# Kernel optimization log

Hardware: AMD Instinct MI355X
Metric: run time of the kernel (lower is better)

Reference implementation:

```python
import math
import jax, jax.numpy as jnp
import numpy as np

NUM_HEADS = 4
HEAD_DIM = 384


def reshape_fortran(x, shape):
    # column-major (Fortran) reshape, matching the torch reverse-permute trick
    x = jnp.transpose(x, tuple(reversed(range(x.ndim))))
    x = x.reshape(tuple(reversed(shape)))
    return jnp.transpose(x, tuple(reversed(range(len(shape)))))


def rel_pos_rotate(data):
    # data: [b, n_heads, L=2M-1, S] -> [b, n_heads, S, S]
    data = jnp.transpose(data, (0, 2, 3, 1))  # [b, d0=L, d1=S, d2=H]
    b, d0, d1, d2 = data.shape
    data = jnp.concatenate([data, jnp.zeros((b, d1, d1, d2), data.dtype)], axis=1)
    data = reshape_fortran(data, (b, (d0 + d1) * d1, 1, d2))
    data = data[:, :(d1 + d0 - 1) * d1]
    data = reshape_fortran(data, (b, d0 + d1 - 1, d1, d2))
    n = d0 // 2
    data = jnp.swapaxes(data[:, n:n + d1], 1, 2)  # [b, d1, d1, d2]
    return jnp.transpose(data, (0, 3, 1, 2))      # [b, H, S, S]


def setup_inputs() -> dict:
    key = jax.random.key(0)
    ks = jax.random.split(key, 5)
    B, S, D = 4, 920, 1536
    M = 920
    return {
        "hidden_states": jax.random.normal(ks[0], (B, S, D), jnp.float32),
        "q_w": jax.random.normal(ks[1], (D, NUM_HEADS * HEAD_DIM), jnp.float32) * 0.02,
        "k_w": jax.random.normal(ks[2], (D, NUM_HEADS * HEAD_DIM), jnp.float32) * 0.02,
        "v_w": jax.random.normal(ks[3], (D, NUM_HEADS * HEAD_DIM), jnp.float32) * 0.02,
        "dist_emb": jax.random.normal(ks[4], (2 * M - 1, HEAD_DIM), jnp.float32) * 0.02,
    }


def reference(hidden_states, q_w, k_w, v_w, dist_emb):
    B, S, D = hidden_states.shape

    def heads(x):  # [B,S,H*hd] -> [B,H,S,hd]
        return jnp.transpose(x.reshape(B, S, NUM_HEADS, HEAD_DIM), (0, 2, 1, 3))

    # query is pre-scaled by 1/sqrt(head_dim), matching the torch code
    q = heads((hidden_states @ q_w) / math.sqrt(HEAD_DIM))
    k = heads(hidden_states @ k_w)
    v = heads(hidden_states @ v_w)

    scores = jnp.einsum("bhqd,bhkd->bhqk", q, k)  # [B,H,S,S]
    # relative position scores: [B,H,L,S] then skew-rotated into [B,H,S,S]
    rel = jnp.einsum("ld,bhsd->bhls", dist_emb, q)
    scores = scores + rel_pos_rotate(rel)

    probs = jax.nn.softmax(scores, axis=-1)
    ctx = jnp.einsum("bhqk,bhkd->bhqd", probs, v)  # [B,H,S,hd]
    ctx = jnp.transpose(ctx, (0, 2, 1, 3)).reshape(B, S, NUM_HEADS * HEAD_DIM)
    return ctx
```

## Files before the change

### kernel.cpp

```cpp
#include <hip/hip_runtime.h>
#include <cstdint>
#include <cstddef>

#define SEQ   920
#define DM    1536
#define DH    384
#define NHD   4
#define NB    4
#define NBH   16
#define MTOK  3680
#define NREL  1839

typedef short          bf16x8 __attribute__((ext_vector_type(8)));
typedef float          f32x4  __attribute__((ext_vector_type(4)));
typedef unsigned short u16x4  __attribute__((ext_vector_type(4)));
typedef unsigned short u16x8  __attribute__((ext_vector_type(8)));

__device__ __forceinline__ unsigned short f2bf(float f){
  union{float f; unsigned u;} v; v.f = f;
  unsigned r = v.u + 0x7FFFu + ((v.u >> 16) & 1u);
  return (unsigned short)(r >> 16);
}
__device__ __forceinline__ float bf2f(unsigned short h){
  union{unsigned u; float f;} v; v.u = ((unsigned)h) << 16;
  return v.f;
}
__device__ __forceinline__ f32x4 mfma_bf16(bf16x8 a, bf16x8 b, f32x4 c){
  return __builtin_amdgcn_mfma_f32_16x16x32_bf16(a, b, c, 0, 0, 0);
}
__device__ __forceinline__ void gload_lds16(const void* g, void* l){
  __builtin_amdgcn_global_load_lds((const __attribute__((address_space(1))) void*)g,
                                   (__attribute__((address_space(3))) void*)l, 16, 0, 0);
}

__global__ __launch_bounds__(256) void k_prep(const float* __restrict__ X,
                                              const float* __restrict__ de,
                                              const float* __restrict__ qw,
                                              const float* __restrict__ kw,
                                              const float* __restrict__ vw,
                                              unsigned short* __restrict__ Xb,
                                              unsigned short* __restrict__ Eb,
                                              unsigned short* __restrict__ Wt){
  __shared__ float t[32][33];
  int bid = blockIdx.x;
  if(bid < 6912){
    int z = bid / 2304, rem = bid % 2304;
    int k0 = (rem % 48) * 32, n0 = (rem / 48) * 32;
    const float* w = z == 0 ? qw : (z == 1 ? kw : vw);
    int tx = threadIdx.x & 31, ty = threadIdx.x >> 5;
    #pragma unroll
    for(int j = 0; j < 4; j++)
      t[ty*4+j][tx] = w[(size_t)(k0 + ty*4 + j) * DM + n0 + tx];
    __syncthreads();
    #pragma unroll
    for(int j = 0; j < 4; j++)
      Wt[(size_t)(z*DM + n0 + ty*4 + j) * DM + k0 + tx] = f2bf(t[tx][ty*4+j]);
  } else if(bid < 6912 + 2048){
    int i = ((bid - 6912) * 256 + threadIdx.x) * 4;
    const int n = MTOK*DM, stride = 2048 * 256 * 4;
    for(; i + 3 < n; i += stride){
      f32x4 v = *(const f32x4*)(X + i);
      u16x4 o; o.x = f2bf(v.x); o.y = f2bf(v.y); o.z = f2bf(v.z); o.w = f2bf(v.w);
      *(u16x4*)(Xb + i) = o;
    }
  } else {
    int i = ((bid - 6912 - 2048) * 256 + threadIdx.x) * 4;
    if(i + 3 < NREL*DH){
      f32x4 v = *(const f32x4*)(de + i);
      u16x4 o; o.x = f2bf(v.x); o.y = f2bf(v.y); o.z = f2bf(v.z); o.w = f2bf(v.w);
      *(u16x4*)(Eb + i) = o;
    }
  }
}

template<class Epi>
__device__ __forceinline__ void gemm384(const unsigned short* __restrict__ A, int lda, int Amax,
                                        const unsigned short* __restrict__ B, int ldb, int Bmax,
                                        int K, int m0, int n0, Epi epi){
  __shared__ char lds[147456];
  char* ldsA = lds;
  char* ldsB = lds + 98304;
  const int tid = threadIdx.x;
  const int w = tid >> 6, l = tid & 63;
  const int lg = l >> 4, lo = l & 15;
  const int wm = w >> 1, wn = w & 1;

  const int gcol = ((tid & 7) ^ ((tid >> 3) & 7)) * 16;
  const char* gA[6]; const char* gB[3];
  #pragma unroll
  for(int u = 0; u < 6; u++){
    int ar = m0 + u*64 + (tid >> 3); ar = ar < Amax ? ar : Amax - 1;
    gA[u] = (const char*)A + (size_t)ar*lda*2 + gcol;
  }
  #pragma unroll
  for(int v = 0; v < 3; v++){
    int br = n0 + v*64 + (tid >> 3); br = br < Bmax ? br : Bmax - 1;
    gB[v] = (const char*)B + (size_t)br*ldb*2 + gcol;
  }
  auto stA = [&](int kt, int s, int u){
    gload_lds16(gA[u] + (size_t)kt*128, ldsA + s*49152 + u*8192 + tid*16);
  };
  auto stB = [&](int kt, int s, int v){
    gload_lds16(gB[v] + (size_t)kt*128, ldsB + s*24576 + v*8192 + tid*16);
  };

  f32x4 acc[6][6] = {};
  const int sw = (lo & 7) << 4;
  const int nk = K >> 6;

  stA(0,0,0); stA(0,0,1); stA(0,0,3); stA(0,0,4);
  stB(0,0,0); stB(0,0,1); stB(0,0,2);
  stA(0,0,2); stA(0,0,5);
  asm volatile("s_waitcnt vmcnt(2)" ::: "memory");
  __builtin_amdgcn_s_barrier();

  for(int t = 0; t < nk; t++){
    const int s = t & 1, sn = s ^ 1;
    const bool pf = (t + 1 < nk);
    const char* Ab = ldsA + s*49152;
    const char* Bb = ldsB + s*24576;
    bf16x8 bfr[6][2], af[2][2];

    #pragma unroll
    for(int fj = 0; fj < 6; fj++){
      int row = wn*96 + fj*16 + lo;
      #pragma unroll
      for(int kk = 0; kk < 2; kk++)
        bfr[fj][kk] = *(const bf16x8*)(Bb + row*128 + ((kk*64 + lg*16) ^ sw));
    }
    #pragma unroll
    for(int fi = 0; fi < 2; fi++){
      int row = wm*96 + fi*16 + lo;
      #pragma unroll
      for(int kk = 0; kk < 2; kk++)
        af[fi][kk] = *(const bf16x8*)(Ab + row*128 + ((kk*64 + lg*16) ^ sw));
    }
    if(pf){ stA(t+1,sn,0); stA(t+1,sn,1); stA(t+1,sn,3);
            asm volatile("s_waitcnt vmcnt(3)" ::: "memory"); }
    else  { asm volatile("s_waitcnt vmcnt(0)" ::: "memory"); }
    __builtin_amdgcn_s_barrier();
    asm volatile("s_waitcnt lgkmcnt(0)" ::: "memory");
    __builtin_amdgcn_s_setprio(1);
    #pragma unroll
    for(int kk = 0; kk < 2; kk++)
      #pragma unroll
      for(int fi = 0; fi < 2; fi++)
        #pragma unroll
        for(int fj = 0; fj < 6; fj++)
          acc[fi][fj] = mfma_bf16(af[fi][kk], bfr[fj][kk], acc[fi][fj]);
    __builtin_amdgcn_s_setprio(0);

    #pragma unroll
    for(int fi = 0; fi < 2; fi++){
      int row = wm*96 + (fi + 2)*16 + lo;
      #pragma unroll
      for(int kk = 0; kk < 2; kk++)
        af[fi][kk] = *(const bf16x8*)(Ab + row*128 + ((kk*64 + lg*16) ^ sw));
    }
    if(pf){ stA(t+1,sn,4); stB(t+1,sn,0); stB(t+1,sn,1); }
    __builtin_amdgcn_s_barrier();
    asm volatile("s_waitcnt lgkmcnt(0)" ::: "memory");
    __builtin_amdgcn_s_setprio(1);
    #pragma unroll
    for(int kk = 0; kk < 2; kk++)
      #pragma unroll
      for(int fi = 0; fi < 2; fi++)
        #pragma unroll
        for(int fj = 0; fj < 6; fj++)
          acc[fi + 2][fj] = mfma_bf16(af[fi][kk], bfr[fj][kk], acc[fi + 2][fj]);
    __builtin_amdgcn_s_setprio(0);

    #pragma unroll
    for(int fi = 0; fi < 2; fi++){
      int row = wm*96 + (fi + 4)*16 + lo;
      #pragma unroll
      for(int kk = 0; kk < 2; kk++)
        af[fi][kk] = *(const bf16x8*)(Ab + row*128 + ((kk*64 + lg*16) ^ sw));
    }
    if(pf){ stB(t+1,sn,2); stA(t+1,sn,2); stA(t+1,sn,5);
            asm volatile("s_waitcnt vmcnt(2)" ::: "memory"); }
    __builtin_amdgcn_s_barrier();
    asm volatile("s_waitcnt lgkmcnt(0)" ::: "memory");
    __builtin_amdgcn_s_setprio(1);
    #pragma unroll
    for(int kk = 0; kk < 2; kk++)
      #pragma unroll
      for(int fi = 0; fi < 2; fi++)
        #pragma unroll
        for(int fj = 0; fj < 6; fj++)
          acc[fi + 4][fj] = mfma_bf16(af[fi][kk], bfr[fj][kk], acc[fi + 4][fj]);
    __builtin_amdgcn_s_setprio(0);
  }

  #pragma unroll
  for(int fi = 0; fi < 6; fi++)
    #pragma unroll
    for(int fj = 0; fj < 6; fj++){
      int m = m0 + wm*96 + fi*16 + lg*4;
      int n = n0 + wn*96 + fj*16 + lo;
      epi(m, n, acc[fi][fj]);
    }
}

template<class Epi>
__device__ __forceinline__ void gemm192(const unsigned short* __restrict__ A, int lda, int Amax,
                                        const unsigned short* __restrict__ B, int ldb, int Bmax,
                                        int K, int m0, int n0, Epi epi){
  __shared__ unsigned short As[3*192*64];
  __shared__ unsigned short Bs[3*192*64];
  const int tid = threadIdx.x;
  const int w = tid >> 6, l = tid & 63;
  const int lg = l >> 4, lo = l & 15;
  const int wm = w >> 2, wn = w & 3;

  const char* ga[3]; const char* gb[3];
  #pragma unroll
  for(int r = 0; r < 3; r++){
    int row = r*64 + (tid >> 3);
    int gslot = (tid & 7) ^ (row & 7);
    int ar = m0 + row; ar = ar < Amax ? ar : Amax - 1;
    ga[r] = (const char*)A + (size_t)ar*lda*2 + gslot*16;
    int br = n0 + row; br = br < Bmax ? br : Bmax - 1;
    gb[r] = (const char*)B + (size_t)br*ldb*2 + gslot*16;
  }
  const int ldst = tid * 16;

  auto stage_pair = [&](int kt, int slot, int r){
    size_t koff = (size_t)kt * 128;
    gload_lds16(ga[r] + koff, (char*)As + slot*24576 + r*8192 + ldst);
    gload_lds16(gb[r] + koff, (char*)Bs + slot*24576 + r*8192 + ldst);
  };

  f32x4 acc[6][3] = {};
  const int sw = (lo & 7) << 4;
  const int nk = (2*K + 127) >> 7;
  const int tb = 2*K - (nk - 1)*128;
  const bool keep0 = (lg*16) < tb;
  const bool keep1 = (64 + lg*16) < tb;

  #pragma unroll
  for(int r = 0; r < 3; r++) stage_pair(0, 0, r);
  #pragma unroll
  for(int r = 0; r < 3; r++) stage_pair(1, 1, r);
  asm volatile("s_waitcnt vmcnt(6)" ::: "memory");
  __builtin_amdgcn_s_barrier();

  int st = 0;
  for(int t = 0; t < nk; t++){
    const bool last = (t == nk - 1);
    const bool pf = (t + 2 < nk);
    const int s2 = st + 2 >= 3 ? st - 1 : st + 2;
    const char* Ab = (const char*)As + st*24576;
    const char* Bb = (const char*)Bs + st*24576;

    bf16x8 bfr[3][2], afr[2][2];

    #pragma unroll
    for(int fj = 0; fj < 3; fj++){
      int row = wn*48 + fj*16 + lo;
      #pragma unroll
      for(int kk = 0; kk < 2; kk++)
        bfr[fj][kk] = *(const bf16x8*)(Bb + row*128 + ((kk*64 + lg*16) ^ sw));
    }
    #pragma unroll
    for(int fi = 0; fi < 2; fi++){
      int row = wm*96 + fi*16 + lo;
      #pragma unroll
      for(int kk = 0; kk < 2; kk++)
        afr[fi][kk] = *(const bf16x8*)(Ab + row*128 + ((kk*64 + lg*16) ^ sw));
    }
    if(pf) stage_pair(t + 2, s2, 0);
    if(last){
      #pragma unroll
      for(int fi = 0; fi < 2; fi++){
        if(!keep0) afr[fi][0] = bf16x8{};
        if(!keep1) afr[fi][1] = bf16x8{};
      }
    }
    __builtin_amdgcn_s_barrier();
    asm volatile("s_waitcnt lgkmcnt(0)" ::: "memory");
    __builtin_amdgcn_s_setprio(1);
    #pragma unroll
    for(int kk = 0; kk < 2; kk++)
      #pragma unroll
      for(int fi = 0; fi < 2; fi++)
        #pragma unroll
        for(int fj = 0; fj < 3; fj++)
          acc[fi][fj] = mfma_bf16(afr[fi][kk], bfr[fj][kk], acc[fi][fj]);
    __builtin_amdgcn_s_setprio(0);
    __builtin_amdgcn_s_barrier();

    #pragma unroll
    for(int fi = 0; fi < 2; fi++){
      int row = wm*96 + (fi + 2)*16 + lo;
      #pragma unroll
      for(int kk = 0; kk < 2; kk++)
        afr[fi][kk] = *(const bf16x8*)(Ab + row*128 + ((kk*64 + lg*16) ^ sw));
    }
    if(pf) stage_pair(t + 2, s2, 1);
    if(last){
      #pragma unroll
      for(int fi = 0; fi < 2; fi++){
        if(!keep0) afr[fi][0] = bf16x8{};
        if(!keep1) afr[fi][1] = bf16x8{};
      }
    }
    __builtin_amdgcn_s_barrier();
    asm volatile("s_waitcnt lgkmcnt(0)" ::: "memory");
    __builtin_amdgcn_s_setprio(1);
    #pragma unroll
    for(int kk = 0; kk < 2; kk++)
      #pragma unroll
      for(int fi = 0; fi < 2; fi++)
        #pragma unroll
        for(int fj = 0; fj < 3; fj++)
          acc[fi + 2][fj] = mfma_bf16(afr[fi][kk], bfr[fj][kk], acc[fi + 2][fj]);
    __builtin_amdgcn_s_setprio(0);
    __builtin_amdgcn_s_barrier();

    #pragma unroll
    for(int fi = 0; fi < 2; fi++){
      int row = wm*96 + (fi + 4)*16 + lo;
      #pragma unroll
      for(int kk = 0; kk < 2; kk++)
        afr[fi][kk] = *(const bf16x8*)(Ab + row*128 + ((kk*64 + lg*16) ^ sw));
    }
    if(pf){
      stage_pair(t + 2, s2, 2);
      asm volatile("s_waitcnt vmcnt(6)" ::: "memory");
    } else if(t + 1 < nk){
      asm volatile("s_waitcnt vmcnt(0)" ::: "memory");
    }
    if(last){
      #pragma unroll
      for(int fi = 0; fi < 2; fi++){
        if(!keep0) afr[fi][0] = bf16x8{};
        if(!keep1) afr[fi][1] = bf16x8{};
      }
    }
    __builtin_amdgcn_s_barrier();
    asm volatile("s_waitcnt lgkmcnt(0)" ::: "memory");
    __builtin_amdgcn_s_setprio(1);
    #pragma unroll
    for(int kk = 0; kk < 2; kk++)
      #pragma unroll
      for(int fi = 0; fi < 2; fi++)
        #pragma unroll
        for(int fj = 0; fj < 3; fj++)
          acc[fi + 4][fj] = mfma_bf16(afr[fi][kk], bfr[fj][kk], acc[fi + 4][fj]);
    __builtin_amdgcn_s_setprio(0);
    __builtin_amdgcn_s_barrier();

    st = st + 1 >= 3 ? 0 : st + 1;
  }

  #pragma unroll
  for(int fi = 0; fi < 6; fi++)
    #pragma unroll
    for(int fj = 0; fj < 3; fj++){
      int m = m0 + wm*96 + fi*16 + lg*4;
      int n = n0 + wn*48 + fj*16 + lo;
      epi(m, n, acc[fi][fj]);
    }
}

template<class Epi>
__device__ __forceinline__ void gemm256(const unsigned short* __restrict__ A, int lda, int Amax,
                                        const unsigned short* __restrict__ B, int ldb, int Bmax,
                                        int K, int m0, int n0, Epi epi){
  __shared__ char lds[131072];
  char* ldsA = lds;
  char* ldsB = lds + 65536;
  const int tid = threadIdx.x;
  const int w = tid >> 6, l = tid & 63;
  const int lg = l >> 4, lo = l & 15;
  const int wm = w >> 2, wn = w & 3;

  const int gcol = ((tid & 7) ^ ((tid >> 3) & 7)) * 16;
  const char* gA[2][2]; const char* gB[2][2];
  #pragma unroll
  for(int u = 0; u < 2; u++)
    #pragma unroll
    for(int j = 0; j < 2; j++){
      int ar = m0 + u*128 + j*64 + (tid >> 3); ar = ar < Amax ? ar : Amax - 1;
      gA[u][j] = (const char*)A + (size_t)ar*lda*2 + gcol;
      int br = n0 + u*128 + j*64 + (tid >> 3); br = br < Bmax ? br : Bmax - 1;
      gB[u][j] = (const char*)B + (size_t)br*ldb*2 + gcol;
    }
  auto stageA = [&](int kt, int s, int u){
    size_t koff = (size_t)kt * 128;
    #pragma unroll
    for(int j = 0; j < 2; j++)
      gload_lds16(gA[u][j] + koff, ldsA + s*32768 + u*16384 + j*8192 + tid*16);
  };
  auto stageB = [&](int kt, int s, int u){
    size_t koff = (size_t)kt * 128;
    #pragma unroll
    for(int j = 0; j < 2; j++)
      gload_lds16(gB[u][j] + koff, ldsB + s*32768 + u*16384 + j*8192 + tid*16);
  };

  f32x4 acc[2][4][4] = {};
  const int sw = (lo & 7) << 4;
  const int nk = K >> 6;

  stageB(0, 0, 0); stageB(0, 0, 1); stageA(0, 0, 0); stageA(0, 0, 1);
  asm volatile("s_waitcnt vmcnt(2)" ::: "memory");
  __builtin_amdgcn_s_barrier();

  for(int t = 0; t < nk; t++){
    const int s = t & 1, sn = s ^ 1;
    const bool pf = (t + 1 < nk);
    const char* Ab = ldsA + s*32768;
    const char* Bb = ldsB + s*32768;
    bf16x8 b0[4], b1[4], ar[4];

    #pragma unroll
    for(int fj = 0; fj < 4; fj++)
      b0[fj] = *(const bf16x8*)(Bb + (wn*64 + fj*16 + lo)*128 + ((lg*16) ^ sw));
    #pragma unroll
    for(int fi = 0; fi < 4; fi++)
      ar[fi] = *(const bf16x8*)(Ab + (wm*64 + fi*16 + lo)*128 + ((lg*16) ^ sw));
    if(pf) stageB(t + 1, sn, 0);
    __builtin_amdgcn_s_barrier();
    asm volatile("s_waitcnt lgkmcnt(0)" ::: "memory");
    __builtin_amdgcn_s_setprio(1);
    #pragma unroll
    for(int fi = 0; fi < 4; fi++)
      #pragma unroll
      for(int fj = 0; fj < 4; fj++)
        acc[0][fi][fj] = mfma_bf16(ar[fi], b0[fj], acc[0][fi][fj]);
    __builtin_amdgcn_s_setprio(0);

    #pragma unroll
    for(int fj = 0; fj < 4; fj++)
      b1[fj] = *(const bf16x8*)(Bb + (wn*64 + fj*16 + lo)*128 + ((64 + lg*16) ^ sw));
    #pragma unroll
    for(int fi = 0; fi < 4; fi++)
      ar[fi] = *(const bf16x8*)(Ab + (wm*64 + fi*16 + lo)*128 + ((64 + lg*16) ^ sw));
    if(pf){ stageB(t + 1, sn, 1);
            asm volatile("s_waitcnt vmcnt(4)" ::: "memory"); }
    else  { asm volatile("s_waitcnt vmcnt(0)" ::: "memory"); }
    __builtin_amdgcn_s_barrier();
    asm volatile("s_waitcnt lgkmcnt(0)" ::: "memory");
    __builtin_amdgcn_s_setprio(1);
    #pragma unroll
    for(int fi = 0; fi < 4; fi++)
      #pragma unroll
      for(int fj = 0; fj < 4; fj++)
        acc[0][fi][fj] = mfma_bf16(ar[fi], b1[fj], acc[0][fi][fj]);
    __builtin_amdgcn_s_setprio(0);

    #pragma unroll
    for(int fi = 0; fi < 4; fi++)
      ar[fi] = *(const bf16x8*)(Ab + (128 + wm*64 + fi*16 + lo)*128 + ((lg*16) ^ sw));
    if(pf) stageA(t + 1, sn, 0);
    __builtin_amdgcn_s_barrier();
    asm volatile("s_waitcnt lgkmcnt(0)" ::: "memory");
    __builtin_amdgcn_s_setprio(1);
    #pragma unroll
    for(int fi = 0; fi < 4; fi++)
      #pragma unroll
      for(int fj = 0; fj < 4; fj++)
        acc[1][fi][fj] = mfma_bf16(ar[fi], b0[fj], acc[1][fi][fj]);
    __builtin_amdgcn_s_setprio(0);

    #pragma unroll
    for(int fi = 0; fi < 4; fi++)
      ar[fi] = *(const bf16x8*)(Ab + (128 + wm*64 + fi*16 + lo)*128 + ((64 + lg*16) ^ sw));
    if(pf){ stageA(t + 1, sn, 1);
            asm volatile("s_waitcnt vmcnt(2)" ::: "memory"); }
    __builtin_amdgcn_s_barrier();
    asm volatile("s_waitcnt lgkmcnt(0)" ::: "memory");
    __builtin_amdgcn_s_setprio(1);
    #pragma unroll
    for(int fi = 0; fi < 4; fi++)
      #pragma unroll
      for(int fj = 0; fj < 4; fj++)
        acc[1][fi][fj] = mfma_bf16(ar[fi], b1[fj], acc[1][fi][fj]);
    __builtin_amdgcn_s_setprio(0);
  }

  #pragma unroll
  for(int lh = 0; lh < 2; lh++)
    #pragma unroll
    for(int fi = 0; fi < 4; fi++)
      #pragma unroll
      for(int fj = 0; fj < 4; fj++){
        int m = m0 + lh*128 + wm*64 + fi*16 + lg*4;
        int n = n0 + wn*64 + fj*16 + lo;
        epi(m, n, acc[lh][fi][fj]);
      }
}

__global__ __launch_bounds__(512, 2) void k_proj(const unsigned short* __restrict__ X,
                                                 const unsigned short* __restrict__ Wt,
                                                 unsigned short* __restrict__ Qb,
                                                 unsigned short* __restrict__ Kb,
                                                 unsigned short* __restrict__ Vt){
  int bid = blockIdx.x;
  int wg  = (bid & 7) * 30 + (bid >> 3);
  int m0 = (wg % 10) * 384, n0 = (wg / 10) * 192;
  gemm384(X, DM, MTOK, Wt, DM, 3*DM, DM, m0, n0,
    [=] __device__ (int m, int n, f32x4 v4){
      if(m >= MTOK) return;
      int which = n / DM, r = n % DM, h = r / DH, d = r % DH;
      int b = m / SEQ, s = m % SEQ;
      int bh = b * NHD + h;
      if(which == 2){
        u16x4 o;
        o.x = f2bf(v4.x); o.y = f2bf(v4.y); o.z = f2bf(v4.z); o.w = f2bf(v4.w);
        *(u16x4*)(Vt + ((size_t)bh*DH + d)*SEQ + s) = o;
      } else if(which == 0){
        #pragma unroll
        for(int i = 0; i < 4; i++)
          Qb[((size_t)bh*SEQ + s + i)*DH + d] = f2bf(v4[i] * 0.05103103630798287f);
      } else {
        #pragma unroll
        for(int i = 0; i < 4; i++)
          Kb[((size_t)bh*SEQ + s + i)*DH + d] = f2bf(v4[i]);
      }
    });
}

__global__ __launch_bounds__(512) void k_rel(const unsigned short* __restrict__ Qb,
                                             const unsigned short* __restrict__ E,
                                             unsigned short* __restrict__ relS){
  int m0 = blockIdx.x * 192, n0 = blockIdx.y * 192;
  int s0 = m0 % SEQ;
  int qlo = s0, qhi = s0 + 191;
  if(qhi >= SEQ){ qlo = 0; qhi = SEQ - 1; }
  if(n0 + 191 < 919 - qhi || n0 > 1838 - qlo) return;
  gemm192(Qb, DH, NBH*SEQ, E, DH, NREL, DH, m0, n0,
    [=] __device__ (int m, int n, f32x4 v4){
      #pragma unroll
      for(int i = 0; i < 4; i++){
        int mi = m + i;
        if(mi >= NBH*SEQ) continue;
        int q = mi % SEQ;
        int j = n - 919 + q;
        if(j < 0 || j >= SEQ) continue;
        relS[(size_t)mi*SEQ + j] = f2bf(v4[i]);
      }
    });
}

__global__ __launch_bounds__(512, 2) void k_sgemm(const unsigned short* __restrict__ Qb,
                                                  const unsigned short* __restrict__ Kb,
                                                  unsigned short* __restrict__ P,
                                                  float* __restrict__ rs2){
  __shared__ float rsLds[256];
  if(threadIdx.x < 256) rsLds[threadIdx.x] = 0.f;
  int bid = blockIdx.x;
  int wg = (bid & 7) * 32 + (bid >> 3);
  int bh = wg >> 4, r = wg & 15;
  int m0 = (r & 3) * 256, n0 = (r >> 2) * 256;
  const unsigned short* A = Qb + (size_t)bh*SEQ*DH;
  const unsigned short* B = Kb + (size_t)bh*SEQ*DH;
  unsigned short* Pbh = P + (size_t)bh*SEQ*SEQ;
  const int lo = threadIdx.x & 15;
  gemm256(A, DH, SEQ, B, DH, SEQ, DH, m0, n0,
    [=] __device__ (int m, int n, f32x4 v4){
      float s[4];
      #pragma unroll
      for(int i = 0; i < 4; i++){
        int mi = m + i;
        float p = 0.f;
        if(mi < SEQ && n < SEQ){
          size_t off = (size_t)mi*SEQ + n;
          p = __expf(v4[i] + bf2f(Pbh[off]));
          Pbh[off] = f2bf(p);
        }
        s[i] = p;
      }
      #pragma unroll
      for(int i = 0; i < 4; i++){
        float v = s[i];
        v += __shfl_xor(v, 1); v += __shfl_xor(v, 2);
        v += __shfl_xor(v, 4); v += __shfl_xor(v, 8);
        if(lo == 0) atomicAdd(&rsLds[m - m0 + i], v);
      }
    });
  __syncthreads();
  if(threadIdx.x < 256){
    int row = m0 + threadIdx.x;
    if(row < SEQ) rs2[(((size_t)(n0 >> 8))*NBH + bh)*SEQ + row] = rsLds[threadIdx.x];
  }
}

__global__ __launch_bounds__(512) void k_pv(const unsigned short* __restrict__ P,
                                            const unsigned short* __restrict__ Vt,
                                            const float* __restrict__ rs2,
                                            float* __restrict__ out){
  int bid = blockIdx.x;
  int idp = (bid & 7) * 20 + (bid >> 3);
  int bh = idp / 10, r = idp % 10;
  int m0 = (r % 5) * 192, n0 = (r / 5) * 192;
  const unsigned short* A = P  + (size_t)bh*SEQ*SEQ;
  const unsigned short* B = Vt + (size_t)bh*DH*SEQ;
  const int b = bh >> 2, h = bh & 3;
  gemm192(A, SEQ, SEQ, B, SEQ, DH, SEQ, m0, n0,
    [=] __device__ (int m, int n, f32x4 v4){
      #pragma unroll
      for(int i = 0; i < 4; i++){
        int mi = m + i;
        if(mi >= SEQ) continue;
        float den = rs2[(size_t)bh*SEQ + mi]
                  + rs2[((size_t)1*NBH + bh)*SEQ + mi]
                  + rs2[((size_t)2*NBH + bh)*SEQ + mi]
                  + rs2[((size_t)3*NBH + bh)*SEQ + mi];
        out[((size_t)(b*SEQ + mi))*DM + h*DH + n] = v4[i] / den;
      }
    });
}

extern "C" void kernel_launch(void* const* d_in, const int* in_sizes, int n_in,
                              void* d_out, int out_size, void* d_ws, size_t ws_size,
                              hipStream_t stream){
  const float* X  = (const float*)d_in[0];
  const float* qw = (const float*)d_in[1];
  const float* kw = (const float*)d_in[2];
  const float* vw = (const float*)d_in[3];
  const float* de = (const float*)d_in[4];
  float* out = (float*)d_out;
  char* ws = (char*)d_ws;

  unsigned short* Qb   = (unsigned short*)ws;
  unsigned short* Kb   = (unsigned short*)(ws + 11304960);
  unsigned short* Vt   = (unsigned short*)(ws + 22609920);
  unsigned short* relS = (unsigned short*)(ws + 33914880);
  unsigned short* Eb   = (unsigned short*)(ws + 60999680);
  unsigned short* Xb   = (unsigned short*)(ws + 33914880);
  unsigned short* Wt   = (unsigned short*)(ws + 45219840);
  float*          rs2  = (float*)(ws + 60999680);

  k_prep<<<dim3(9650), dim3(256), 0, stream>>>(X, de, qw, kw, vw, Xb, Eb, Wt);
  k_proj<<<dim3(240), dim3(512), 0, stream>>>(Xb, Wt, Qb, Kb, Vt);
  k_rel<<<dim3(77,10), dim3(512), 0, stream>>>(Qb, Eb, relS);
  k_sgemm<<<dim3(256), dim3(512), 0, stream>>>(Qb, Kb, relS, rs2);
  k_pv<<<dim3(160), dim3(512), 0, stream>>>(relS, Vt, rs2, out);
}
```

Measured before the change: 210.2 us.

## Simplify GEMM main loop to bulk prefetch and two MFMA phases

Replaces the three-phase GEMM inner loop, which interleaved partial global-to-LDS prefetches with partial vmcnt waits and barriers, with a simpler schedule. Each iteration now issues every next-tile load up front, then runs two MFMA phases of three A fragments each, and ends with one full vmcnt wait and a barrier. The aim is to cut barrier and synchronisation overhead and give the loads a whole iteration to complete. In exchange it holds more fragment registers live and loses the fine-grained staggering of load issue against compute.

```diff
diff --git a/kernel.cpp b/kernel.cpp
--- a/kernel.cpp
+++ b/kernel.cpp
@@ -97,21 +97,22 @@
     int br = n0 + v*64 + (tid >> 3); br = br < Bmax ? br : Bmax - 1;
     gB[v] = (const char*)B + (size_t)br*ldb*2 + gcol;
   }
-  auto stA = [&](int kt, int s, int u){
-    gload_lds16(gA[u] + (size_t)kt*128, ldsA + s*49152 + u*8192 + tid*16);
-  };
-  auto stB = [&](int kt, int s, int v){
-    gload_lds16(gB[v] + (size_t)kt*128, ldsB + s*24576 + v*8192 + tid*16);
+  auto stage_all = [&](int kt, int s){
+    size_t koff = (size_t)kt * 128;
+    #pragma unroll
+    for(int u = 0; u < 6; u++)
+      gload_lds16(gA[u] + koff, ldsA + s*49152 + u*8192 + tid*16);
+    #pragma unroll
+    for(int v = 0; v < 3; v++)
+      gload_lds16(gB[v] + koff, ldsB + s*24576 + v*8192 + tid*16);
   };
 
   f32x4 acc[6][6] = {};
   const int sw = (lo & 7) << 4;
   const int nk = K >> 6;
 
-  stA(0,0,0); stA(0,0,1); stA(0,0,3); stA(0,0,4);
-  stB(0,0,0); stB(0,0,1); stB(0,0,2);
-  stA(0,0,2); stA(0,0,5);
-  asm volatile("s_waitcnt vmcnt(2)" ::: "memory");
+  stage_all(0, 0);
+  asm volatile("s_waitcnt vmcnt(0)" ::: "memory");
   __builtin_amdgcn_s_barrier();
 
   for(int t = 0; t < nk; t++){
@@ -119,77 +120,54 @@
     const bool pf = (t + 1 < nk);
     const char* Ab = ldsA + s*49152;
     const char* Bb = ldsB + s*24576;
-    bf16x8 bfr[6][2], af[2][2];
-
+    if(pf) stage_all(t + 1, sn);
+
+    bf16x8 b0[6], b1[6], a0[3], a1[3];
     #pragma unroll
     for(int fj = 0; fj < 6; fj++){
-      int row = wn*96 + fj*16 + lo;
-      #pragma unroll
-      for(int kk = 0; kk < 2; kk++)
-        bfr[fj][kk] = *(const bf16x8*)(Bb + row*128 + ((kk*64 + lg*16) ^ sw));
-    }
-    #pragma unroll
-    for(int fi = 0; fi < 2; fi++){
-      int row = wm*96 + fi*16 + lo;
-      #pragma unroll
-      for(int kk = 0; kk < 2; kk++)
-        af[fi][kk] = *(const bf16x8*)(Ab + row*128 + ((kk*64 + lg*16) ^ sw));
-    }
-    if(pf){ stA(t+1,sn,0); stA(t+1,sn,1); stA(t+1,sn,3);
-            asm volatile("s_waitcnt vmcnt(3)" ::: "memory"); }
-    else  { asm volatile("s_waitcnt vmcnt(0)" ::: "memory"); }
-    __builtin_amdgcn_s_barrier();
-    asm volatile("s_waitcnt lgkmcnt(0)" ::: "memory");
-    __builtin_amdgcn_s_setprio(1);
-    #pragma unroll
-    for(int kk = 0; kk < 2; kk++)
-      #pragma unroll
-      for(int fi = 0; fi < 2; fi++)
-        #pragma unroll
-        for(int fj = 0; fj < 6; fj++)
-          acc[fi][fj] = mfma_bf16(af[fi][kk], bfr[fj][kk], acc[fi][fj]);
-    __builtin_amdgcn_s_setprio(0);
-
-    #pragma unroll
-    for(int fi = 0; fi < 2; fi++){
-      int row = wm*96 + (fi + 2)*16 + lo;
-      #pragma unroll
-      for(int kk = 0; kk < 2; kk++)
-        af[fi][kk] = *(const bf16x8*)(Ab + row*128 + ((kk*64 + lg*16) ^ sw));
-    }
-    if(pf){ stA(t+1,sn,4); stB(t+1,sn,0); stB(t+1,sn,1); }
-    __builtin_amdgcn_s_barrier();
-    asm volatile("s_waitcnt lgkmcnt(0)" ::: "memory");
-    __builtin_amdgcn_s_setprio(1);
-    #pragma unroll
-    for(int kk = 0; kk < 2; kk++)
-      #pragma unroll
-      for(int fi = 0; fi < 2; fi++)
-        #pragma unroll
-        for(int fj = 0; fj < 6; fj++)
-          acc[fi + 2][fj] = mfma_bf16(af[fi][kk], bfr[fj][kk], acc[fi + 2][fj]);
-    __builtin_amdgcn_s_setprio(0);
-
-    #pragma unroll
-    for(int fi = 0; fi < 2; fi++){
-      int row = wm*96 + (fi + 4)*16 + lo;
-      #pragma unroll
-      for(int kk = 0; kk < 2; kk++)
-        af[fi][kk] = *(const bf16x8*)(Ab + row*128 + ((kk*64 + lg*16) ^ sw));
-    }
-    if(pf){ stB(t+1,sn,2); stA(t+1,sn,2); stA(t+1,sn,5);
-            asm volatile("s_waitcnt vmcnt(2)" ::: "memory"); }
-    __builtin_amdgcn_s_barrier();
-    asm volatile("s_waitcnt lgkmcnt(0)" ::: "memory");
-    __builtin_amdgcn_s_setprio(1);
-    #pragma unroll
-    for(int kk = 0; kk < 2; kk++)
-      #pragma unroll
-      for(int fi = 0; fi < 2; fi++)
-        #pragma unroll
-        for(int fj = 0; fj < 6; fj++)
-          acc[fi + 4][fj] = mfma_bf16(af[fi][kk], bfr[fj][kk], acc[fi + 4][fj]);
-    __builtin_amdgcn_s_setprio(0);
+      b0[fj] = *(const bf16x8*)(Bb + (wn*96 + fj*16 + lo)*128 + ((lg*16) ^ sw));
+      b1[fj] = *(const bf16x8*)(Bb + (wn*96 + fj*16 + lo)*128 + ((64 + lg*16) ^ sw));
+    }
+    #pragma unroll
+    for(int fi = 0; fi < 3; fi++){
+      a0[fi] = *(const bf16x8*)(Ab + (wm*96 + fi*16 + lo)*128 + ((lg*16) ^ sw));
+      a1[fi] = *(const bf16x8*)(Ab + (wm*96 + fi*16 + lo)*128 + ((64 + lg*16) ^ sw));
+    }
+    __builtin_amdgcn_s_setprio(1);
+    #pragma unroll
+    for(int fi = 0; fi < 3; fi++)
+      #pragma unroll
+      for(int fj = 0; fj < 6; fj++)
+        acc[fi][fj] = mfma_bf16(a0[fi], b0[fj], acc[fi][fj]);
+    #pragma unroll
+    for(int fi = 0; fi < 3; fi++)
+      #pragma unroll
+      for(int fj = 0; fj < 6; fj++)
+        acc[fi][fj] = mfma_bf16(a1[fi], b1[fj], acc[fi][fj]);
+    __builtin_amdgcn_s_setprio(0);
+
+    #pragma unroll
+    for(int fi = 0; fi < 3; fi++){
+      a0[fi] = *(const bf16x8*)(Ab + (wm*96 + (fi+3)*16 + lo)*128 + ((lg*16) ^ sw));
+      a1[fi] = *(const bf16x8*)(Ab + (wm*96 + (fi+3)*16 + lo)*128 + ((64 + lg*16) ^ sw));
+    }
+    __builtin_amdgcn_s_setprio(1);
+    #pragma unroll
+    for(int fi = 0; fi < 3; fi++)
+      #pragma unroll
+      for(int fj = 0; fj < 6; fj++)
+        acc[fi+3][fj] = mfma_bf16(a0[fi], b0[fj], acc[fi+3][fj]);
+    #pragma unroll
+    for(int fi = 0; fi < 3; fi++)
+      #pragma unroll
+      for(int fj = 0; fj < 6; fj++)
+        acc[fi+3][fj] = mfma_bf16(a1[fi], b1[fj], acc[fi+3][fj]);
+    __builtin_amdgcn_s_setprio(0);
+
+    if(pf){
+      asm volatile("s_waitcnt vmcnt(0)" ::: "memory");
+      __builtin_amdgcn_s_barrier();
+    }
   }
 
   #pragma unroll
```

Result: no change. 208.7 us (-0.7%).
